# Kernel optimization log

Hardware: AMD Instinct MI355X
Metric: run time of the kernel (lower is better)

The kernel has to match this reference:

```python
import jax, jax.numpy as jnp
import numpy as np

B, S, D = 4, 2048, 1024  # batch, seq_len, d_model (h=16 but unused due to source bug)


def setup_inputs() -> dict:
    key = jax.random.key(0)
    ks = jax.random.split(key, 12)
    scale = 1.0 / np.sqrt(D)
    return {
        "q": jax.random.normal(ks[0], (B, S, D), jnp.float32),
        "k": jax.random.normal(ks[1], (B, S, D), jnp.float32),
        "v": jax.random.normal(ks[2], (B, S, D), jnp.float32),
        "mask": jnp.ones((1, 1, S, S), dtype=bool),
        "Wq": jax.random.normal(ks[3], (D, D), jnp.float32) * scale,
        "bq": jnp.zeros((D,), jnp.float32),
        "Wk": jax.random.normal(ks[4], (D, D), jnp.float32) * scale,
        "bk": jnp.zeros((D,), jnp.float32),
        "Wv": jax.random.normal(ks[5], (D, D), jnp.float32) * scale,
        "bv": jnp.zeros((D,), jnp.float32),
        "Wo": jax.random.normal(ks[6], (D, D), jnp.float32) * scale,
        "bo": jnp.zeros((D,), jnp.float32),
    }


def reference(q, k, v, mask, Wq, bq, Wk, bk, Wv, bv, Wo, bo):
    # Faithful to source bugs: head split discarded (attention over full d_model),
    # mask discarded (masked_fill out-of-place), dropout=0 (identity).
    query = q @ Wq + bq  # [B,S,D]
    key = k @ Wk + bk
    value = v @ Wv + bv
    d_k = query.shape[-1]  # = d_model due to the bug
    scores = jnp.einsum('bqd,bkd->bqk', query, key) / jnp.sqrt(jnp.float32(d_k))
    attn = jax.nn.softmax(scores, axis=-1)  # [B,S,S]
    x = jnp.einsum('bqk,bkd->bqd', attn, value)  # [B,S,D]
    # source: x.transpose(1,2).contiguous().view(B,-1,D) -> layout permutation
    b, s, d = x.shape
    x = jnp.swapaxes(x, 1, 2).reshape(b, s, d)
    return x @ Wo + bo
```

## Files before the change

### kernel.cpp

```cpp
#include <hip/hip_runtime.h>
#include <hip/hip_bf16.h>
#include <stdint.h>

typedef __attribute__((ext_vector_type(8))) short short8;
typedef __attribute__((ext_vector_type(4))) float f32x4;
typedef __attribute__((ext_vector_type(16))) float f32x16;
typedef const __attribute__((address_space(1))) uint32_t* gas1_t;
typedef __attribute__((address_space(3))) uint32_t* las3_t;

__device__ __forceinline__ short f2bf(float f) {
  uint32_t u = __builtin_bit_cast(uint32_t, f);
  u += 0x7fffu + ((u >> 16) & 1u);
  return (short)(u >> 16);
}
__device__ __forceinline__ float bf2f(short s) {
  return __builtin_bit_cast(float, ((uint32_t)(uint16_t)s) << 16);
}

__global__ __launch_bounds__(256) void cvt_qkv_k(const float* __restrict__ q,
    const float* __restrict__ k, const float* __restrict__ v,
    short* __restrict__ dst) {
  const long long n = 8388608LL;
  const float* src = (blockIdx.z == 0) ? q : (blockIdx.z == 1) ? k : v;
  long long i = ((long long)blockIdx.x * 256 + threadIdx.x) * 8;
  float4 a = *(const float4*)(src + i);
  float4 b = *(const float4*)(src + i + 4);
  short8 o;
  o[0]=f2bf(a.x); o[1]=f2bf(a.y); o[2]=f2bf(a.z); o[3]=f2bf(a.w);
  o[4]=f2bf(b.x); o[5]=f2bf(b.y); o[6]=f2bf(b.z); o[7]=f2bf(b.w);
  *(short8*)(dst + (long long)blockIdx.z * n + i) = o;
}

__global__ __launch_bounds__(256) void bias_gather_k(const float* b0, const float* b1,
    const float* b2, const float* b3, float* __restrict__ dst) {
  int i = blockIdx.x * 256 + threadIdx.x;
  if (i >= 4096) return;
  int z = i >> 10, j = i & 1023;
  const float* s = (z==0)?b0:(z==1)?b1:(z==2)?b2:b3;
  dst[i] = s[j];
}

__global__ __launch_bounds__(256) void wt_cvt_k(const float* w0, const float* w1,
    const float* w2, const float* w3, short* __restrict__ dst) {
  __shared__ float t[32][33];
  const float* W = (blockIdx.z==0)?w0:(blockIdx.z==1)?w1:(blockIdx.z==2)?w2:w3;
  short* D = dst + (long long)blockIdx.z * 1048576LL;
  int n0 = blockIdx.x * 32, k0 = blockIdx.y * 32;
  int tx = threadIdx.x, ty = threadIdx.y;
  #pragma unroll
  for (int i = 0; i < 4; ++i)
    t[ty + 8*i][tx] = W[(long long)(k0 + ty + 8*i) * 1024 + n0 + tx];
  __syncthreads();
  #pragma unroll
  for (int i = 0; i < 4; ++i)
    D[(long long)(n0 + ty + 8*i) * 1024 + k0 + tx] = f2bf(t[tx][ty + 8*i]);
}

__global__ __launch_bounds__(256) void softmax_bf_k(short* __restrict__ SP) {
  short* sp = SP + (long long)blockIdx.x * 2048;
  const int t = threadIdx.x;
  short8 sv = *(const short8*)(sp + t*8);
  float v[8];
  #pragma unroll
  for (int j = 0; j < 8; ++j) v[j] = bf2f(sv[j]);
  float m = v[0];
  #pragma unroll
  for (int j = 1; j < 8; ++j) m = fmaxf(m, v[j]);
  #pragma unroll
  for (int off = 32; off > 0; off >>= 1) m = fmaxf(m, __shfl_down(m, off, 64));
  __shared__ float rmax[4], rsum[4];
  int wv = t >> 6, ln = t & 63;
  if (ln == 0) rmax[wv] = m;
  __syncthreads();
  m = fmaxf(fmaxf(rmax[0], rmax[1]), fmaxf(rmax[2], rmax[3]));
  float e[8], sum = 0.f;
  #pragma unroll
  for (int j = 0; j < 8; ++j) { e[j] = exp2f((v[j] - m) * 1.44269504f); sum += e[j]; }
  #pragma unroll
  for (int off = 32; off > 0; off >>= 1) sum += __shfl_down(sum, off, 64);
  if (ln == 0) rsum[wv] = sum;
  __syncthreads();
  float inv = 1.0f / (rsum[0] + rsum[1] + rsum[2] + rsum[3]);
  short8 o;
  #pragma unroll
  for (int j = 0; j < 8; ++j) o[j] = f2bf(e[j] * inv);
  *(short8*)(sp + t*8) = o;
}

#define MFMA16(d, a_, b_) d = __builtin_amdgcn_mfma_f32_16x16x32_bf16(a_, b_, d, 0, 0, 0)
#define MFMA32(d, a_, b_) d = __builtin_amdgcn_mfma_f32_32x32x16_bf16(a_, b_, d, 0, 0, 0)
#define LGKM0 do { asm volatile("s_waitcnt lgkmcnt(0)" ::: "memory"); \
                   __builtin_amdgcn_sched_barrier(0); } while (0)
#define XCD_DECODE(gxs_, gys_) \
  const int nwg = (int)gridDim.x; \
  const int wg = ((int)blockIdx.x & 7) * (nwg >> 3) + ((int)blockIdx.x >> 3); \
  const int bxi = wg & ((1 << (gxs_)) - 1); \
  const int byi = (wg >> (gxs_)) & ((1 << (gys_)) - 1); \
  const int z = wg >> ((gxs_) + (gys_));

template<int OUT_BF16>
__global__ __launch_bounds__(512, 4) void gemm4h_k(const short* __restrict__ A,
    const short* __restrict__ Bt, void* __restrict__ Cv,
    const float* __restrict__ bias,
    int K, int lda, int ldb, int ldc,
    long long sA, long long sB, long long sC, long long sBias,
    float scale, int gxs, int gys)
{
  __shared__ __align__(16) short lds[3][12288];
  XCD_DECODE(gxs, gys);
  A  += (long long)z * sA;
  Bt += (long long)z * sB;
  const int bm = byi * 256;
  const int bn = bxi * 128;
  const int tid  = threadIdx.x;
  const int w    = tid >> 6, lane = tid & 63;
  const int wr   = w >> 1,   wc   = w & 1;
  const int lr   = lane & 15, lk  = lane >> 4;

  const int rsw  = (lk ^ ((lr >> 1) & 3)) * 8;
  const int srow = w * 16 + (lane >> 2);
  const int sg   = ((lane & 3) ^ ((lane >> 3) & 3)) * 8;
  const short* gA[2]; const short* gB;
  #pragma unroll
  for (int h = 0; h < 2; ++h)
    gA[h] = A + (long long)(bm + h*128 + srow) * lda + sg;
  gB = Bt + (long long)(bn + srow) * ldb + sg;

  #define STGAh(buf, h, kt) \
    __builtin_amdgcn_global_load_lds((gas1_t)(gA[h] + (long long)(kt)*32), \
        (las3_t)&lds[buf][(h)*4096 + w*512], 16, 0, 0)
  #define STGBh(buf, kt) \
    __builtin_amdgcn_global_load_lds((gas1_t)(gB + (long long)(kt)*32), \
        (las3_t)&lds[buf][8192 + w*512], 16, 0, 0)
  #define RDAh(buf, mi) (*(const short8*)&lds[buf][(wr*64 + (mi)*16 + lr)*32 + rsw])
  #define RDBh(buf, ni) (*(const short8*)&lds[buf][8192 + (wc*64 + (ni)*16 + lr)*32 + rsw])

  f32x4 acc[4][4] = {};
  const int nt = K >> 5;

  STGAh(0, 0, 0); STGAh(0, 1, 0); STGBh(0, 0);
  STGAh(1, 0, 1); STGAh(1, 1, 1); STGBh(1, 1);
  asm volatile("s_waitcnt vmcnt(3)" ::: "memory");
  __builtin_amdgcn_s_barrier();

  int b = 0, nb = 2;
  for (int g = 0; g < nt; ++g) {
    short8 aR[4], bR[4];
    #pragma unroll
    for (int mi = 0; mi < 4; ++mi) aR[mi] = RDAh(b, mi);
    #pragma unroll
    for (int ni = 0; ni < 4; ++ni) bR[ni] = RDBh(b, ni);
    if (g + 2 < nt) { STGAh(nb, 0, g+2); STGAh(nb, 1, g+2); STGBh(nb, g+2); }
    LGKM0;
    __builtin_amdgcn_s_setprio(1);
    #pragma unroll
    for (int mi = 0; mi < 4; ++mi)
      #pragma unroll
      for (int ni = 0; ni < 4; ++ni)
        MFMA16(acc[mi][ni], aR[mi], bR[ni]);
    __builtin_amdgcn_s_setprio(0);
    if (g + 2 < nt)      asm volatile("s_waitcnt vmcnt(3)" ::: "memory");
    else if (g + 1 < nt) asm volatile("s_waitcnt vmcnt(0)" ::: "memory");
    __builtin_amdgcn_s_barrier();
    b  = (b  == 2) ? 0 : b  + 1;
    nb = (nb == 2) ? 0 : nb + 1;
  }

  const float* bz = bias ? (bias + (long long)z * sBias) : nullptr;
  #pragma unroll
  for (int mi = 0; mi < 4; ++mi) {
    const int row = bm + wr*64 + mi*16 + lk*4;
    #pragma unroll
    for (int ni = 0; ni < 4; ++ni) {
      const int col = bn + wc*64 + ni*16 + lr;
      const float bval = bz ? bz[col] : 0.f;
      #pragma unroll
      for (int r = 0; r < 4; ++r) {
        float val = acc[mi][ni][r] * scale + bval;
        if (OUT_BF16)
          ((short*)Cv)[(long long)z*sC + (long long)(row + r) * ldc + col] = f2bf(val);
        else
          ((float*)Cv)[(long long)z*sC + (long long)(row + r) * ldc + col] = val;
      }
    }
  }
  #undef STGAh
  #undef STGBh
  #undef RDAh
  #undef RDBh
}

template<int OUT_BF16, int BIAS_ROW>
__global__ __launch_bounds__(512, 2) void gemm4_k(const short* __restrict__ A,
    const short* __restrict__ Bt, void* __restrict__ Cv,
    const float* __restrict__ bias,
    int K, int lda, int ldb, int ldc,
    long long sA, long long sB, long long sC, long long sBias,
    float scale, int gxs, int gys)
{
  __shared__ __align__(16) short lds[3][24576];
  XCD_DECODE(gxs, gys);
  A  += (long long)z * sA;
  Bt += (long long)z * sB;
  const int bm = byi * 256;
  const int bn = bxi * 128;
  const int tid  = threadIdx.x;
  const int w    = tid >> 6, lane = tid & 63;
  const int wr   = w >> 1,   wc   = w & 1;
  const int l31  = lane & 31, l5 = lane >> 5, rq = lane & 7;

  const int srow = w * 8 + (lane >> 3);
  const int swc  = ((lane & 7) ^ ((lane >> 3) & 7)) * 8;
  const short* gA[4]; const short* gB[2];
  #pragma unroll
  for (int i = 0; i < 4; ++i)
    gA[i] = A + (long long)(bm + i*64 + srow) * lda + swc;
  #pragma unroll
  for (int i = 0; i < 2; ++i)
    gB[i] = Bt + (long long)(bn + i*64 + srow) * ldb + swc;

  #define STGA(buf, i, kt) \
    __builtin_amdgcn_global_load_lds((gas1_t)(gA[i] + (long long)(kt)*64), \
        (las3_t)&lds[buf][(i)*4096 + w*512], 16, 0, 0)
  #define STGB(buf, i, kt) \
    __builtin_amdgcn_global_load_lds((gas1_t)(gB[i] + (long long)(kt)*64), \
        (las3_t)&lds[buf][16384 + (i)*4096 + w*512], 16, 0, 0)
  #define RDA32(buf, mi, ks) (*(const short8*)&lds[buf][(wr*64 + (mi)*32 + l31)*64 + ((((ks)*2 + l5) ^ rq))*8])
  #define RDB32(buf, ni, ks) (*(const short8*)&lds[buf][16384 + (wc*64 + (ni)*32 + l31)*64 + ((((ks)*2 + l5) ^ rq))*8])

  f32x16 acc[2][2] = {};
  const int nt = K >> 6;

  STGA(0, 0, 0); STGA(0, 2, 0); STGB(0, 0, 0);
  STGB(0, 1, 0); STGA(0, 1, 0); STGA(0, 3, 0);
  STGA(1, 0, 1); STGA(1, 2, 1); STGB(1, 0, 1);
  STGB(1, 1, 1); STGA(1, 1, 1); STGA(1, 3, 1);
  asm volatile("s_waitcnt vmcnt(6)" ::: "memory");
  __builtin_amdgcn_s_barrier();

  int b = 0, nb = 2;
  for (int g = 0; g < nt; ++g) {
    short8 aR[2][2], bR[2][2];
    #pragma unroll
    for (int mi = 0; mi < 2; ++mi) { aR[mi][0] = RDA32(b, mi, 0); aR[mi][1] = RDA32(b, mi, 1); }
    #pragma unroll
    for (int ni = 0; ni < 2; ++ni) { bR[ni][0] = RDB32(b, ni, 0); bR[ni][1] = RDB32(b, ni, 1); }
    if (g + 2 < nt) { STGA(nb, 0, g+2); STGA(nb, 2, g+2); STGB(nb, 0, g+2); }
    LGKM0;
    __builtin_amdgcn_s_setprio(1);
    #pragma unroll
    for (int mi = 0; mi < 2; ++mi)
      #pragma unroll
      for (int ni = 0; ni < 2; ++ni) {
        MFMA32(acc[mi][ni], aR[mi][0], bR[ni][0]);
        MFMA32(acc[mi][ni], aR[mi][1], bR[ni][1]);
      }
    __builtin_amdgcn_s_setprio(0);
    #pragma unroll
    for (int mi = 0; mi < 2; ++mi) { aR[mi][0] = RDA32(b, mi, 2); aR[mi][1] = RDA32(b, mi, 3); }
    #pragma unroll
    for (int ni = 0; ni < 2; ++ni) { bR[ni][0] = RDB32(b, ni, 2); bR[ni][1] = RDB32(b, ni, 3); }
    if (g + 2 < nt) { STGB(nb, 1, g+2); STGA(nb, 1, g+2); STGA(nb, 3, g+2); }
    LGKM0;
    __builtin_amdgcn_s_setprio(1);
    #pragma unroll
    for (int mi = 0; mi < 2; ++mi)
      #pragma unroll
      for (int ni = 0; ni < 2; ++ni) {
        MFMA32(acc[mi][ni], aR[mi][0], bR[ni][0]);
        MFMA32(acc[mi][ni], aR[mi][1], bR[ni][1]);
      }
    __builtin_amdgcn_s_setprio(0);
    if (g + 2 < nt)      asm volatile("s_waitcnt vmcnt(6)" ::: "memory");
    else if (g + 1 < nt) asm volatile("s_waitcnt vmcnt(0)" ::: "memory");
    __builtin_amdgcn_s_barrier();
    b  = (b  == 2) ? 0 : b  + 1;
    nb = (nb == 2) ? 0 : nb + 1;
  }

  const float* bz = bias;
  #pragma unroll
  for (int mi = 0; mi < 2; ++mi) {
    #pragma unroll
    for (int ni = 0; ni < 2; ++ni) {
      const int col = bn + wc*64 + ni*32 + l31;
      const float bcol = (bz && !BIAS_ROW) ? bz[(long long)z*sBias + col] : 0.f;
      #pragma unroll
      for (int r = 0; r < 16; ++r) {
        const int row = bm + wr*64 + mi*32 + (r&3) + 8*(r>>2) + 4*l5;
        float bval = BIAS_ROW ? bz[row] : bcol;
        float val = acc[mi][ni][r] * scale + bval;
        if (OUT_BF16)
          ((short*)Cv)[(long long)z*sC + (long long)row * ldc + col] = f2bf(val);
        else
          ((float*)Cv)[(long long)z*sC + (long long)row * ldc + col] = val;
      }
    }
  }
  #undef STGA
  #undef STGB
  #undef RDA32
  #undef RDB32
}

extern "C" void kernel_launch(void* const* d_in, const int* in_sizes, int n_in,
                              void* d_out, int out_size, void* d_ws, size_t ws_size,
                              hipStream_t stream) {
  const float* q  = (const float*)d_in[0];
  const float* k  = (const float*)d_in[1];
  const float* v  = (const float*)d_in[2];
  const float* Wq = (const float*)d_in[4];
  const float* bq = (const float*)d_in[5];
  const float* Wk = (const float*)d_in[6];
  const float* bk = (const float*)d_in[7];
  const float* Wv = (const float*)d_in[8];
  const float* bv = (const float*)d_in[9];
  const float* Wo = (const float*)d_in[10];
  const float* bo = (const float*)d_in[11];

  char* w = (char*)d_ws;
  short* Wt     = (short*)(w);
  float* biasb  = (float*)(w + 8388608);
  short* QKV    = (short*)(w + 8404992);
  short* qkvbf  = (short*)(w + 58736640);
  short* P      = (short*)(w + 58736640);
  short* Vt     = (short*)(w + 109068288);
  short* xt     = (short*)(w + 125845504);

  short* Qp = QKV;
  short* Kp = QKV + 8388608LL;
  short* vbf = qkvbf + 16777216LL;

  cvt_qkv_k<<<dim3(4096,1,3), 256, 0, stream>>>(q, k, v, qkvbf);
  bias_gather_k<<<dim3(16), 256, 0, stream>>>(bq, bk, bv, bo, biasb);
  wt_cvt_k<<<dim3(32,32,4), dim3(32,8), 0, stream>>>(Wq, Wk, Wv, Wo, Wt);

  gemm4h_k<1><<<512, 512, 0, stream>>>(qkvbf, Wt, QKV, biasb,
      1024, 1024, 1024, 1024, 8388608LL, 1048576LL, 8388608LL, 1024LL, 1.0f, 3, 5);

  gemm4_k<1,1><<<256, 512, 0, stream>>>(Wt + 2097152LL, vbf, Vt, biasb + 2048,
      1024, 1024, 1024, 8192, 0LL, 0LL, 0LL, 0LL, 1.0f, 6, 2);

  gemm4h_k<1><<<512, 512, 0, stream>>>(Qp, Kp, P, nullptr,
      1024, 1024, 1024, 2048, 2097152LL, 2097152LL, 4194304LL, 0LL, 0.03125f, 4, 3);

  softmax_bf_k<<<dim3(8192), 256, 0, stream>>>(P);

  gemm4_k<1,0><<<256, 512, 0, stream>>>(Vt, P, xt, nullptr,
      2048, 8192, 2048, 2048, 2048LL, 4194304LL, 2097152LL, 0LL, 1.0f, 4, 2);

  gemm4_k<0,0><<<256, 512, 0, stream>>>(xt, Wt + 3145728LL, (float*)d_out,
      biasb + 3072, 1024, 1024, 1024, 1024, 2097152LL, 0LL, 2097152LL, 0LL, 1.0f, 3, 3);
}
```

Before: 219.2 us.

## Enlarge QK/QKV GEMM tiles to 256x256 and switch gemm4 to 16x16 MFMA

The half-K GEMM used for the Q/K projections and the QK^T scores now computes a 256x256 tile per workgroup instead of 256x128. Each wave does 8x4 16x16 MFMA fragments, and the global-to-LDS loads are split across two compute phases. This halves the number of workgroups and raises operand reuse per loaded byte, at the cost of more accumulator registers and lower occupancy (launch bounds go from 4 to 2). Separately, the 64-K GEMM replaces its 32x32x16 MFMAs with 16x16x32 MFMAs, using a new LDS swizzle and a new epilogue indexing.

```diff
diff --git a/kernel.cpp b/kernel.cpp
--- a/kernel.cpp
+++ b/kernel.cpp
@@ -4,7 +4,6 @@
 
 typedef __attribute__((ext_vector_type(8))) short short8;
 typedef __attribute__((ext_vector_type(4))) float f32x4;
-typedef __attribute__((ext_vector_type(16))) float f32x16;
 typedef const __attribute__((address_space(1))) uint32_t* gas1_t;
 typedef __attribute__((address_space(3))) uint32_t* las3_t;
 
@@ -88,7 +87,6 @@
 }
 
 #define MFMA16(d, a_, b_) d = __builtin_amdgcn_mfma_f32_16x16x32_bf16(a_, b_, d, 0, 0, 0)
-#define MFMA32(d, a_, b_) d = __builtin_amdgcn_mfma_f32_32x32x16_bf16(a_, b_, d, 0, 0, 0)
 #define LGKM0 do { asm volatile("s_waitcnt lgkmcnt(0)" ::: "memory"); \
                    __builtin_amdgcn_sched_barrier(0); } while (0)
 #define XCD_DECODE(gxs_, gys_) \
@@ -99,58 +97,59 @@
   const int z = wg >> ((gxs_) + (gys_));
 
 template<int OUT_BF16>
-__global__ __launch_bounds__(512, 4) void gemm4h_k(const short* __restrict__ A,
+__global__ __launch_bounds__(512, 2) void gemm2_k(const short* __restrict__ A,
     const short* __restrict__ Bt, void* __restrict__ Cv,
     const float* __restrict__ bias,
     int K, int lda, int ldb, int ldc,
     long long sA, long long sB, long long sC, long long sBias,
     float scale, int gxs, int gys)
 {
-  __shared__ __align__(16) short lds[3][12288];
+  __shared__ __align__(16) short lds[3][16384];
   XCD_DECODE(gxs, gys);
   A  += (long long)z * sA;
   Bt += (long long)z * sB;
   const int bm = byi * 256;
-  const int bn = bxi * 128;
+  const int bn = bxi * 256;
   const int tid  = threadIdx.x;
   const int w    = tid >> 6, lane = tid & 63;
-  const int wr   = w >> 1,   wc   = w & 1;
+  const int wr   = w >> 2,   wc   = w & 3;
   const int lr   = lane & 15, lk  = lane >> 4;
 
   const int rsw  = (lk ^ ((lr >> 1) & 3)) * 8;
   const int srow = w * 16 + (lane >> 2);
   const int sg   = ((lane & 3) ^ ((lane >> 3) & 3)) * 8;
-  const short* gA[2]; const short* gB;
-  #pragma unroll
-  for (int h = 0; h < 2; ++h)
-    gA[h] = A + (long long)(bm + h*128 + srow) * lda + sg;
-  gB = Bt + (long long)(bn + srow) * ldb + sg;
-
-  #define STGAh(buf, h, kt) \
-    __builtin_amdgcn_global_load_lds((gas1_t)(gA[h] + (long long)(kt)*32), \
-        (las3_t)&lds[buf][(h)*4096 + w*512], 16, 0, 0)
-  #define STGBh(buf, kt) \
-    __builtin_amdgcn_global_load_lds((gas1_t)(gB + (long long)(kt)*32), \
-        (las3_t)&lds[buf][8192 + w*512], 16, 0, 0)
-  #define RDAh(buf, mi) (*(const short8*)&lds[buf][(wr*64 + (mi)*16 + lr)*32 + rsw])
-  #define RDBh(buf, ni) (*(const short8*)&lds[buf][8192 + (wc*64 + (ni)*16 + lr)*32 + rsw])
-
-  f32x4 acc[4][4] = {};
+  const short* gA[2]; const short* gB[2];
+  #pragma unroll
+  for (int i = 0; i < 2; ++i) {
+    gA[i] = A  + (long long)(bm + i*128 + srow) * lda + sg;
+    gB[i] = Bt + (long long)(bn + i*128 + srow) * ldb + sg;
+  }
+
+  #define STGA2(buf, i, kt) \
+    __builtin_amdgcn_global_load_lds((gas1_t)(gA[i] + (long long)(kt)*32), \
+        (las3_t)&lds[buf][(i)*4096 + w*512], 16, 0, 0)
+  #define STGB2(buf, i, kt) \
+    __builtin_amdgcn_global_load_lds((gas1_t)(gB[i] + (long long)(kt)*32), \
+        (las3_t)&lds[buf][8192 + (i)*4096 + w*512], 16, 0, 0)
+  #define RDA2(buf, mi) (*(const short8*)&lds[buf][(wr*128 + (mi)*16 + lr)*32 + rsw])
+  #define RDB2(buf, ni) (*(const short8*)&lds[buf][8192 + (wc*64 + (ni)*16 + lr)*32 + rsw])
+
+  f32x4 acc[8][4] = {};
   const int nt = K >> 5;
 
-  STGAh(0, 0, 0); STGAh(0, 1, 0); STGBh(0, 0);
-  STGAh(1, 0, 1); STGAh(1, 1, 1); STGBh(1, 1);
-  asm volatile("s_waitcnt vmcnt(3)" ::: "memory");
+  STGA2(0, 0, 0); STGA2(0, 1, 0); STGB2(0, 0, 0); STGB2(0, 1, 0);
+  STGA2(1, 0, 1); STGA2(1, 1, 1); STGB2(1, 0, 1); STGB2(1, 1, 1);
+  asm volatile("s_waitcnt vmcnt(4)" ::: "memory");
   __builtin_amdgcn_s_barrier();
 
   int b = 0, nb = 2;
   for (int g = 0; g < nt; ++g) {
     short8 aR[4], bR[4];
     #pragma unroll
-    for (int mi = 0; mi < 4; ++mi) aR[mi] = RDAh(b, mi);
-    #pragma unroll
-    for (int ni = 0; ni < 4; ++ni) bR[ni] = RDBh(b, ni);
-    if (g + 2 < nt) { STGAh(nb, 0, g+2); STGAh(nb, 1, g+2); STGBh(nb, g+2); }
+    for (int mi = 0; mi < 4; ++mi) aR[mi] = RDA2(b, mi);
+    #pragma unroll
+    for (int ni = 0; ni < 4; ++ni) bR[ni] = RDB2(b, ni);
+    if (g + 2 < nt) { STGA2(nb, 0, g+2); STGA2(nb, 1, g+2); }
     LGKM0;
     __builtin_amdgcn_s_setprio(1);
     #pragma unroll
@@ -159,7 +158,18 @@
       for (int ni = 0; ni < 4; ++ni)
         MFMA16(acc[mi][ni], aR[mi], bR[ni]);
     __builtin_amdgcn_s_setprio(0);
-    if (g + 2 < nt)      asm volatile("s_waitcnt vmcnt(3)" ::: "memory");
+    #pragma unroll
+    for (int mi = 0; mi < 4; ++mi) aR[mi] = RDA2(b, mi + 4);
+    if (g + 2 < nt) { STGB2(nb, 0, g+2); STGB2(nb, 1, g+2); }
+    LGKM0;
+    __builtin_amdgcn_s_setprio(1);
+    #pragma unroll
+    for (int mi = 0; mi < 4; ++mi)
+      #pragma unroll
+      for (int ni = 0; ni < 4; ++ni)
+        MFMA16(acc[mi+4][ni], aR[mi], bR[ni]);
+    __builtin_amdgcn_s_setprio(0);
+    if (g + 2 < nt)      asm volatile("s_waitcnt vmcnt(4)" ::: "memory");
     else if (g + 1 < nt) asm volatile("s_waitcnt vmcnt(0)" ::: "memory");
     __builtin_amdgcn_s_barrier();
     b  = (b  == 2) ? 0 : b  + 1;
@@ -168,8 +178,8 @@
 
   const float* bz = bias ? (bias + (long long)z * sBias) : nullptr;
   #pragma unroll
-  for (int mi = 0; mi < 4; ++mi) {
-    const int row = bm + wr*64 + mi*16 + lk*4;
+  for (int mi = 0; mi < 8; ++mi) {
+    const int row = bm + wr*128 + mi*16 + (lane >> 4)*4;
     #pragma unroll
     for (int ni = 0; ni < 4; ++ni) {
       const int col = bn + wc*64 + ni*16 + lr;
@@ -184,10 +194,10 @@
       }
     }
   }
-  #undef STGAh
-  #undef STGBh
-  #undef RDAh
-  #undef RDBh
+  #undef STGA2
+  #undef STGB2
+  #undef RDA2
+  #undef RDB2
 }
 
 template<int OUT_BF16, int BIAS_ROW>
@@ -207,8 +217,10 @@
   const int tid  = threadIdx.x;
   const int w    = tid >> 6, lane = tid & 63;
   const int wr   = w >> 1,   wc   = w & 1;
-  const int l31  = lane & 31, l5 = lane >> 5, rq = lane & 7;
-
+  const int lr   = lane & 15, lk  = lane >> 4;
+
+  const int rsw0 = ((lk    ) ^ (lr & 7)) * 8;
+  const int rsw1 = ((lk + 4) ^ (lr & 7)) * 8;
   const int srow = w * 8 + (lane >> 3);
   const int swc  = ((lane & 7) ^ ((lane >> 3) & 7)) * 8;
   const short* gA[4]; const short* gB[2];
@@ -225,10 +237,10 @@
   #define STGB(buf, i, kt) \
     __builtin_amdgcn_global_load_lds((gas1_t)(gB[i] + (long long)(kt)*64), \
         (las3_t)&lds[buf][16384 + (i)*4096 + w*512], 16, 0, 0)
-  #define RDA32(buf, mi, ks) (*(const short8*)&lds[buf][(wr*64 + (mi)*32 + l31)*64 + ((((ks)*2 + l5) ^ rq))*8])
-  #define RDB32(buf, ni, ks) (*(const short8*)&lds[buf][16384 + (wc*64 + (ni)*32 + l31)*64 + ((((ks)*2 + l5) ^ rq))*8])
-
-  f32x16 acc[2][2] = {};
+  #define RDA4(buf, mi, ks) (*(const short8*)&lds[buf][(wr*64 + (mi)*16 + lr)*64 + ((ks) ? rsw1 : rsw0)])
+  #define RDB4(buf, ni, ks) (*(const short8*)&lds[buf][16384 + (wc*64 + (ni)*16 + lr)*64 + ((ks) ? rsw1 : rsw0)])
+
+  f32x4 acc[4][4] = {};
   const int nt = K >> 6;
 
   STGA(0, 0, 0); STGA(0, 2, 0); STGB(0, 0, 0);
@@ -240,36 +252,32 @@
 
   int b = 0, nb = 2;
   for (int g = 0; g < nt; ++g) {
-    short8 aR[2][2], bR[2][2];
-    #pragma unroll
-    for (int mi = 0; mi < 2; ++mi) { aR[mi][0] = RDA32(b, mi, 0); aR[mi][1] = RDA32(b, mi, 1); }
-    #pragma unroll
-    for (int ni = 0; ni < 2; ++ni) { bR[ni][0] = RDB32(b, ni, 0); bR[ni][1] = RDB32(b, ni, 1); }
+    short8 aR[4], bR[4];
+    #pragma unroll
+    for (int mi = 0; mi < 4; ++mi) aR[mi] = RDA4(b, mi, 0);
+    #pragma unroll
+    for (int ni = 0; ni < 4; ++ni) bR[ni] = RDB4(b, ni, 0);
     if (g + 2 < nt) { STGA(nb, 0, g+2); STGA(nb, 2, g+2); STGB(nb, 0, g+2); }
     LGKM0;
     __builtin_amdgcn_s_setprio(1);
     #pragma unroll
-    for (int mi = 0; mi < 2; ++mi)
-      #pragma unroll
-      for (int ni = 0; ni < 2; ++ni) {
-        MFMA32(acc[mi][ni], aR[mi][0], bR[ni][0]);
-        MFMA32(acc[mi][ni], aR[mi][1], bR[ni][1]);
-      }
+    for (int mi = 0; mi < 4; ++mi)
+      #pragma unroll
+      for (int ni = 0; ni < 4; ++ni)
+        MFMA16(acc[mi][ni], aR[mi], bR[ni]);
     __builtin_amdgcn_s_setprio(0);
     #pragma unroll
-    for (int mi = 0; mi < 2; ++mi) { aR[mi][0] = RDA32(b, mi, 2); aR[mi][1] = RDA32(b, mi, 3); }
-    #pragma unroll
-    for (int ni = 0; ni < 2; ++ni) { bR[ni][0] = RDB32(b, ni, 2); bR[ni][1] = RDB32(b, ni, 3); }
+    for (int mi = 0; mi < 4; ++mi) aR[mi] = RDA4(b, mi, 1);
+    #pragma unroll
+    for (int ni = 0; ni < 4; ++ni) bR[ni] = RDB4(b, ni, 1);
     if (g + 2 < nt) { STGB(nb, 1, g+2); STGA(nb, 1, g+2); STGA(nb, 3, g+2); }
     LGKM0;
     __builtin_amdgcn_s_setprio(1);
     #pragma unroll
-    for (int mi = 0; mi < 2; ++mi)
-      #pragma unroll
-      for (int ni = 0; ni < 2; ++ni) {
-        MFMA32(acc[mi][ni], aR[mi][0], bR[ni][0]);
-        MFMA32(acc[mi][ni], aR[mi][1], bR[ni][1]);
-      }
+    for (int mi = 0; mi < 4; ++mi)
+      #pragma unroll
+      for (int ni = 0; ni < 4; ++ni)
+        MFMA16(acc[mi][ni], aR[mi], bR[ni]);
     __builtin_amdgcn_s_setprio(0);
     if (g + 2 < nt)      asm volatile("s_waitcnt vmcnt(6)" ::: "memory");
     else if (g + 1 < nt) asm volatile("s_waitcnt vmcnt(0)" ::: "memory");
@@ -280,27 +288,27 @@
 
   const float* bz = bias;
   #pragma unroll
-  for (int mi = 0; mi < 2; ++mi) {
-    #pragma unroll
-    for (int ni = 0; ni < 2; ++ni) {
-      const int col = bn + wc*64 + ni*32 + l31;
+  for (int mi = 0; mi < 4; ++mi) {
+    const int row = bm + wr*64 + mi*16 + lk*4;
+    #pragma unroll
+    for (int ni = 0; ni < 4; ++ni) {
+      const int col = bn + wc*64 + ni*16 + lr;
       const float bcol = (bz && !BIAS_ROW) ? bz[(long long)z*sBias + col] : 0.f;
       #pragma unroll
-      for (int r = 0; r < 16; ++r) {
-        const int row = bm + wr*64 + mi*32 + (r&3) + 8*(r>>2) + 4*l5;
-        float bval = BIAS_ROW ? bz[row] : bcol;
+      for (int r = 0; r < 4; ++r) {
+        float bval = BIAS_ROW ? bz[row + r] : bcol;
         float val = acc[mi][ni][r] * scale + bval;
         if (OUT_BF16)
-          ((short*)Cv)[(long long)z*sC + (long long)row * ldc + col] = f2bf(val);
+          ((short*)Cv)[(long long)z*sC + (long long)(row + r) * ldc + col] = f2bf(val);
         else
-          ((float*)Cv)[(long long)z*sC + (long long)row * ldc + col] = val;
+          ((float*)Cv)[(long long)z*sC + (long long)(row + r) * ldc + col] = val;
       }
     }
   }
   #undef STGA
   #undef STGB
-  #undef RDA32
-  #undef RDB32
+  #undef RDA4
+  #undef RDB4
 }
 
 extern "C" void kernel_launch(void* const* d_in, const int* in_sizes, int n_in,
@@ -335,14 +343,14 @@
   bias_gather_k<<<dim3(16), 256, 0, stream>>>(bq, bk, bv, bo, biasb);
   wt_cvt_k<<<dim3(32,32,4), dim3(32,8), 0, stream>>>(Wq, Wk, Wv, Wo, Wt);
 
-  gemm4h_k<1><<<512, 512, 0, stream>>>(qkvbf, Wt, QKV, biasb,
-      1024, 1024, 1024, 1024, 8388608LL, 1048576LL, 8388608LL, 1024LL, 1.0f, 3, 5);
+  gemm2_k<1><<<256, 512, 0, stream>>>(qkvbf, Wt, QKV, biasb,
+      1024, 1024, 1024, 1024, 8388608LL, 1048576LL, 8388608LL, 1024LL, 1.0f, 2, 5);
 
   gemm4_k<1,1><<<256, 512, 0, stream>>>(Wt + 2097152LL, vbf, Vt, biasb + 2048,
       1024, 1024, 1024, 8192, 0LL, 0LL, 0LL, 0LL, 1.0f, 6, 2);
 
-  gemm4h_k<1><<<512, 512, 0, stream>>>(Qp, Kp, P, nullptr,
-      1024, 1024, 1024, 2048, 2097152LL, 2097152LL, 4194304LL, 0LL, 0.03125f, 4, 3);
+  gemm2_k<1><<<256, 512, 0, stream>>>(Qp, Kp, P, nullptr,
+      1024, 1024, 1024, 2048, 2097152LL, 2097152LL, 4194304LL, 0LL, 0.03125f, 3, 3);
 
   softmax_bf_k<<<dim3(8192), 256, 0, stream>>>(P);
 
```

After: 205.9 us. 6.0% less time.
